# Kernel tuning notes

Hardware: AMD Instinct MI355X
Metric: run time of the kernel (lower is better)

The kernel has to match this reference:

```python
import jax, jax.numpy as jnp
import numpy as np

H, G, K = 8, 2, 16


def _sqdist(a, b):
    # a: [B,N,3], b: [B,M,3] -> [B,N,M] squared euclidean distances
    return ((a * a).sum(-1)[..., None] + (b * b).sum(-1)[..., None, :]
            - 2.0 * jnp.einsum('bnc,bmc->bnm', a, b))


_gather = jax.vmap(lambda p, i: p[i])  # points [N,C], idx [...,] -> [..., C]


def setup_inputs() -> dict:
    key = jax.random.key(0)
    B, N, C = 4, 1024, 384
    ks = jax.random.split(key, 10)
    def w(k, shape):
        return (jax.random.normal(k, shape, jnp.float32) / np.sqrt(shape[0]).astype(np.float32))
    return {
        'q': jax.random.normal(ks[0], (B, N, C), jnp.float32),
        'q_pos': jax.random.normal(ks[1], (B, N, 3), jnp.float32),
        'Wq': w(ks[2], (C, C)), 'Wk': w(ks[3], (C, C)), 'Wv': w(ks[4], (C, C)),
        'Wvoff': w(ks[5], (C, C)),
        'W_off1': w(ks[6], (C, C)),  # in = 2*group_dims = 2*(C//2) = C
        'b_off1': jnp.zeros((C,), jnp.float32),
        'ln_g': jnp.ones((C,), jnp.float32), 'ln_b': jnp.zeros((C,), jnp.float32),
        'W_off2': w(ks[7], (C, 3)),
        'Wp': w(ks[8], (C, C)), 'bp': jnp.zeros((C,), jnp.float32),
    }


def reference(q, q_pos, Wq, Wk, Wv, Wvoff, W_off1, b_off1, ln_g, ln_b, W_off2, Wp, bp):
    B, N, C = q.shape
    hd, gc = C // H, C // G
    scale_attn = hd ** -0.5
    v, v_pos = q, q_pos  # self-attention usage

    # --- kNN in 3D (topk smallest squared distances) ---
    d2 = _sqdist(q_pos, v_pos)                       # [B,N,N]
    _, idx = jax.lax.top_k(-d2, K)                    # [B,N,K]

    qp = q @ Wq                                       # [B,N,C]
    v_off = v @ Wvoff
    local_v = _gather(v_off, idx)                     # [B,N,K,C]

    # group split: 'b n k (g c) -> (b g) n k c'
    off_local_v = local_v.reshape(B, N, K, G, gc).transpose(0, 3, 1, 2, 4).reshape(B * G, N, K, gc)
    group_q = qp.reshape(B, N, G, gc).transpose(0, 2, 1, 3).reshape(B * G, N, gc)
    shift_feat = jnp.concatenate(
        [off_local_v, jnp.broadcast_to(group_q[:, :, None, :], (B * G, N, K, gc))], axis=-1)

    # --- offset MLP: Linear -> LayerNorm -> GELU -> Linear(no bias) -> tanh ---
    h = shift_feat @ W_off1 + b_off1
    mu = h.mean(-1, keepdims=True)
    var = ((h - mu) ** 2).mean(-1, keepdims=True)
    h = (h - mu) / jnp.sqrt(var + 1e-5) * ln_g + ln_b
    h = jax.nn.gelu(h, approximate=False)
    offset = jnp.tanh(h @ W_off2)                     # [(B G),N,K,3]

    # --- shift positions within local ball ---
    local_v_pos = _gather(v_pos, idx)                 # [B,N,K,3]
    local_v_pos = jnp.broadcast_to(local_v_pos[:, None], (B, G, N, K, 3)).reshape(B * G, N, K, 3)
    sc = (local_v_pos.max(-2) - local_v_pos.min(-2))[:, :, None, :] * 0.5
    shift_pos = (local_v_pos + offset * sc).reshape(B * G, N * K, 3)

    v_pos_g = jnp.broadcast_to(v_pos[:, None], (B, G, N, 3)).reshape(B * G, N, 3)
    v_g = v.reshape(B, N, G, gc).transpose(0, 2, 1, 3).reshape(B * G, N, gc)

    # --- three_nn + three_interpolate (inverse-distance weights over 3 NNs) ---
    d2n = _sqdist(shift_pos, v_pos_g)                 # [(B G), N*K, N]
    negd, idx3 = jax.lax.top_k(-d2n, 3)
    dist = jnp.sqrt(jnp.maximum(-negd, 0.0))          # three_nn returns euclidean dist
    recip = 1.0 / (dist + 1e-8)
    weight = recip / recip.sum(-1, keepdims=True)     # [(B G), N*K, 3]
    feats = _gather(v_g, idx3)                        # [(B G), N*K, 3, gc]
    interp = (feats * weight[..., None]).sum(-2)      # [(B G), N*K, gc]
    interp = interp.reshape(B, G, N, K, gc).transpose(0, 2, 3, 1, 4).reshape(B, N, K, C)

    # --- local cross-attn: 1 query token vs K interpolated keys/values ---
    kf = (interp @ Wk).reshape(B, N, K, H, hd)
    vf = (interp @ Wv).reshape(B, N, K, H, hd)
    qh = qp.reshape(B, N, H, hd)
    attn = jnp.einsum('bnhc,bnkhc->bnhk', qh, kf) * scale_attn
    attn = jax.nn.softmax(attn, axis=-1)
    out = jnp.einsum('bnhk,bnkhc->bnhc', attn, vf).reshape(B, N, C)
    return out @ Wp + bp
```

## Files before the change

kernel.cpp:

```cpp
#include <hip/hip_runtime.h>
#include <math.h>


#define ATTN_SCALE 0.14433756729740643f

#define OFF_IDX   0u
#define OFF_SC    65536u
#define OFF_QP    77824u
#define OFF_VOFF  1650688u
#define OFF_P     3223552u
#define OFF_Q     6369280u
#define OFF_SP    9515008u
#define OFF_W3    9908224u
#define OFF_I3    10301440u
#define OFF_QKH   10694656u
#define OFF_VW    23277568u
#define OFF_OPRE  35860480u

__device__ __forceinline__ float fast_erff(float z) {
  float az = fabsf(z);
  float d = fmaf(0.3275911f, az, 1.0f);
  float t0 = __builtin_amdgcn_rcpf(d);
  float t = t0 * fmaf(-d, t0, 2.0f);
  float e = __builtin_amdgcn_exp2f(z * z * -1.4426950408889634f);
  float p = fmaf(fmaf(fmaf(fmaf(1.061405429f, t, -1.453152027f),
                           t, 1.421413741f),
                      t, -0.284496736f),
                 t, 0.254829592f);
  float r = 1.0f - p * t * e;
  return __builtin_copysignf(r, z);
}

__global__ __launch_bounds__(64) void knn_kernel(const float* __restrict__ qpos,
                                                 int* __restrict__ idx_out,
                                                 float* __restrict__ sc_out) {
  int bn = blockIdx.x;
  int b = bn >> 10, n = bn & 1023;
  int lane = threadIdx.x;
  const float* pb = qpos + (size_t)b * 1024 * 3;
  float qx = pb[n * 3 + 0], qy = pb[n * 3 + 1], qz = pb[n * 3 + 2];
  float qq = qx * qx + qy * qy + qz * qz;
  float d2[16];
#pragma unroll
  for (int u = 0; u < 16; ++u) {
    int p = lane + 64 * u;
    float px = pb[p * 3 + 0], py = pb[p * 3 + 1], pz = pb[p * 3 + 2];
    float pp = px * px + py * py + pz * pz;
    float dt = qx * px + qy * py + qz * pz;
    d2[u] = (qq + pp) - 2.0f * dt;
  }
  float mnx = 3.4e38f, mny = 3.4e38f, mnz = 3.4e38f;
  float mxx = -3.4e38f, mxy = -3.4e38f, mxz = -3.4e38f;
  for (int r = 0; r < 16; ++r) {
    float best = d2[0]; int bu = 0;
#pragma unroll
    for (int u = 1; u < 16; ++u) { if (d2[u] < best) { best = d2[u]; bu = u; } }
    int bidx = lane + 64 * bu;
#pragma unroll
    for (int off = 32; off > 0; off >>= 1) {
      float ov = __shfl_xor(best, off);
      int oi = __shfl_xor(bidx, off);
      if (ov < best || (ov == best && oi < bidx)) { best = ov; bidx = oi; }
    }
    if ((bidx & 63) == lane) d2[bidx >> 6] = 3.4e38f;
    float wx = pb[bidx * 3 + 0], wy = pb[bidx * 3 + 1], wz = pb[bidx * 3 + 2];
    mnx = fminf(mnx, wx); mny = fminf(mny, wy); mnz = fminf(mnz, wz);
    mxx = fmaxf(mxx, wx); mxy = fmaxf(mxy, wy); mxz = fmaxf(mxz, wz);
    if (lane == 0) idx_out[bn * 16 + r] = bidx;
  }
  if (lane == 0) {
    sc_out[bn * 3 + 0] = 0.5f * (mxx - mnx);
    sc_out[bn * 3 + 1] = 0.5f * (mxy - mny);
    sc_out[bn * 3 + 2] = 0.5f * (mxz - mnz);
  }
}

__global__ __launch_bounds__(256) void gemm_qp_voff(const float* __restrict__ Aq,
    const float* __restrict__ W1, const float* __restrict__ W2,
    float* __restrict__ O1, float* __restrict__ O2) {
  __shared__ float As[16 * 132];
  __shared__ float Bs1[16 * 64];
  __shared__ float Bs2[16 * 64];
  int tid = threadIdx.x;
  int m0 = blockIdx.x * 128, n0 = blockIdx.y * 64;
  int arow = tid >> 1, akq = (tid & 1) * 8;
  int lk = tid >> 4, ln4 = (tid & 15) * 4;
  int tx = tid & 15, ty = tid >> 4;
  float a11[4][4] = {{0.f}}, a21[4][4] = {{0.f}};
  float a12[4][4] = {{0.f}}, a22[4][4] = {{0.f}};
  for (int k0 = 0; k0 < 384; k0 += 16) {
    float4 a0 = *(const float4*)(Aq + (size_t)(m0 + arow) * 384 + k0 + akq);
    float4 a1 = *(const float4*)(Aq + (size_t)(m0 + arow) * 384 + k0 + akq + 4);
    float4 b1 = *(const float4*)(W1 + (size_t)(k0 + lk) * 384 + n0 + ln4);
    float4 b2 = *(const float4*)(W2 + (size_t)(k0 + lk) * 384 + n0 + ln4);
    __syncthreads();
    As[(akq + 0) * 132 + arow] = a0.x; As[(akq + 1) * 132 + arow] = a0.y;
    As[(akq + 2) * 132 + arow] = a0.z; As[(akq + 3) * 132 + arow] = a0.w;
    As[(akq + 4) * 132 + arow] = a1.x; As[(akq + 5) * 132 + arow] = a1.y;
    As[(akq + 6) * 132 + arow] = a1.z; As[(akq + 7) * 132 + arow] = a1.w;
    *(float4*)(Bs1 + lk * 64 + ln4) = b1;
    *(float4*)(Bs2 + lk * 64 + ln4) = b2;
    __syncthreads();
#pragma unroll
    for (int k = 0; k < 16; ++k) {
      float4 av0 = *(const float4*)(As + k * 132 + ty * 4);
      float4 av1 = *(const float4*)(As + k * 132 + 64 + ty * 4);
      float4 bv1 = *(const float4*)(Bs1 + k * 64 + tx * 4);
      float4 bv2 = *(const float4*)(Bs2 + k * 64 + tx * 4);
      float x0[4] = {av0.x, av0.y, av0.z, av0.w};
      float x1[4] = {av1.x, av1.y, av1.z, av1.w};
      float c1[4] = {bv1.x, bv1.y, bv1.z, bv1.w};
      float c2[4] = {bv2.x, bv2.y, bv2.z, bv2.w};
#pragma unroll
      for (int i = 0; i < 4; ++i)
#pragma unroll
        for (int j = 0; j < 4; ++j) {
          a11[i][j] = fmaf(x0[i], c1[j], a11[i][j]);
          a21[i][j] = fmaf(x1[i], c1[j], a21[i][j]);
          a12[i][j] = fmaf(x0[i], c2[j], a12[i][j]);
          a22[i][j] = fmaf(x1[i], c2[j], a22[i][j]);
        }
    }
  }
#pragma unroll
  for (int i = 0; i < 4; ++i) {
    size_t rA = (size_t)(m0 + ty * 4 + i);
    size_t rB = (size_t)(m0 + 64 + ty * 4 + i);
    *(float4*)(O1 + rA * 384 + n0 + tx * 4) = make_float4(a11[i][0], a11[i][1], a11[i][2], a11[i][3]);
    *(float4*)(O1 + rB * 384 + n0 + tx * 4) = make_float4(a21[i][0], a21[i][1], a21[i][2], a21[i][3]);
    *(float4*)(O2 + rA * 384 + n0 + tx * 4) = make_float4(a12[i][0], a12[i][1], a12[i][2], a12[i][3]);
    *(float4*)(O2 + rB * 384 + n0 + tx * 4) = make_float4(a22[i][0], a22[i][1], a22[i][2], a22[i][3]);
  }
}

__global__ __launch_bounds__(256) void gemm_pq3(const float* __restrict__ voff,
    const float* __restrict__ qp, const float* __restrict__ qin,
    const float* __restrict__ Woff1, const float* __restrict__ boff1,
    const float* __restrict__ Wv,
    float* __restrict__ P, float* __restrict__ Q, float* __restrict__ VW) {
  __shared__ float As[16 * 132];
  __shared__ float Bs[16 * 64];
  int tid = threadIdx.x;
  int m0 = blockIdx.x * 128, n0 = blockIdx.y * 64, z = blockIdx.z;
  int bg = m0 >> 10; int b = bg >> 1; int g = bg & 1; int ml0 = m0 & 1023;
  const float* Abase; const float* Bbase; const float* bias; float* Out; int bog;
  if (z == 0)      { Abase = voff; Bbase = Woff1;             bias = nullptr; Out = P;  bog = 0; }
  else if (z == 1) { Abase = qp;   Bbase = Woff1 + 192 * 384; bias = boff1;   Out = Q;  bog = 0; }
  else             { Abase = qin;  Bbase = Wv;                bias = nullptr; Out = VW; bog = 192 * 384; }
  const float* A = Abase + (size_t)b * 1024 * 384 + g * 192;
  const float* B = Bbase + (size_t)g * bog;
  int arow = tid >> 1, akq = (tid & 1) * 8;
  int lk = tid >> 4, ln4 = (tid & 15) * 4;
  int tx = tid & 15, ty = tid >> 4;
  float accA[4][4] = {{0.f}}, accB[4][4] = {{0.f}};
  for (int k0 = 0; k0 < 192; k0 += 16) {
    float4 a0 = *(const float4*)(A + (size_t)(ml0 + arow) * 384 + k0 + akq);
    float4 a1 = *(const float4*)(A + (size_t)(ml0 + arow) * 384 + k0 + akq + 4);
    float4 b4 = *(const float4*)(B + (size_t)(k0 + lk) * 384 + n0 + ln4);
    __syncthreads();
    As[(akq + 0) * 132 + arow] = a0.x; As[(akq + 1) * 132 + arow] = a0.y;
    As[(akq + 2) * 132 + arow] = a0.z; As[(akq + 3) * 132 + arow] = a0.w;
    As[(akq + 4) * 132 + arow] = a1.x; As[(akq + 5) * 132 + arow] = a1.y;
    As[(akq + 6) * 132 + arow] = a1.z; As[(akq + 7) * 132 + arow] = a1.w;
    *(float4*)(Bs + lk * 64 + ln4) = b4;
    __syncthreads();
#pragma unroll
    for (int k = 0; k < 16; ++k) {
      float4 av0 = *(const float4*)(As + k * 132 + ty * 4);
      float4 av1 = *(const float4*)(As + k * 132 + 64 + ty * 4);
      float4 bv = *(const float4*)(Bs + k * 64 + tx * 4);
      float a0v[4] = {av0.x, av0.y, av0.z, av0.w};
      float a1v[4] = {av1.x, av1.y, av1.z, av1.w};
      float c[4] = {bv.x, bv.y, bv.z, bv.w};
#pragma unroll
      for (int i = 0; i < 4; ++i)
#pragma unroll
        for (int j = 0; j < 4; ++j) {
          accA[i][j] = fmaf(a0v[i], c[j], accA[i][j]);
          accB[i][j] = fmaf(a1v[i], c[j], accB[i][j]);
        }
    }
  }
  float bb[4] = {0.f, 0.f, 0.f, 0.f};
  if (bias) {
    bb[0] = bias[n0 + tx * 4 + 0]; bb[1] = bias[n0 + tx * 4 + 1];
    bb[2] = bias[n0 + tx * 4 + 2]; bb[3] = bias[n0 + tx * 4 + 3];
  }
#pragma unroll
  for (int i = 0; i < 4; ++i) {
    size_t rowA = (size_t)(m0 + ty * 4 + i);
    size_t rowB = (size_t)(m0 + 64 + ty * 4 + i);
    *(float4*)(Out + rowA * 384 + n0 + tx * 4) =
        make_float4(accA[i][0] + bb[0], accA[i][1] + bb[1], accA[i][2] + bb[2], accA[i][3] + bb[3]);
    *(float4*)(Out + rowB * 384 + n0 + tx * 4) =
        make_float4(accB[i][0] + bb[0], accB[i][1] + bb[1], accB[i][2] + bb[2], accB[i][3] + bb[3]);
  }
}

__global__ __launch_bounds__(256) void offset_assemble(const float* __restrict__ P,
    const float* __restrict__ Q, const int* __restrict__ idx,
    const float* __restrict__ lng, const float* __restrict__ lnb,
    const float* __restrict__ W2, const float* __restrict__ qpos,
    const float* __restrict__ sc, float* __restrict__ sp) {
  int row = blockIdx.x * 4 + (threadIdx.x >> 6);
  int lane = threadIdx.x & 63;
  int k = row & 15, n = (row >> 4) & 1023, bg = row >> 14;
  int b = bg >> 1;
  int mi = idx[((b << 10) + n) * 16 + k];
  const float* Pr = P + ((size_t)bg * 1024 + mi) * 384;
  const float* Qr = Q + ((size_t)bg * 1024 + n) * 384;
  float h[6]; float s = 0.f, s2 = 0.f;
#pragma unroll
  for (int u = 0; u < 3; ++u) {
    int c = 2 * lane + 128 * u;
    float2 pv = *(const float2*)(Pr + c);
    float2 qv = *(const float2*)(Qr + c);
    float h0 = pv.x + qv.x, h1 = pv.y + qv.y;
    h[2 * u] = h0; h[2 * u + 1] = h1;
    s += h0 + h1;
    s2 = fmaf(h0, h0, s2);
    s2 = fmaf(h1, h1, s2);
  }
#pragma unroll
  for (int off = 32; off > 0; off >>= 1) {
    s  += __shfl_xor(s, off);
    s2 += __shfl_xor(s2, off);
  }
  float mu = s * (1.0f / 384.0f);
  float var = s2 * (1.0f / 384.0f) - mu * mu;
  float rstd = 1.0f / sqrtf(var + 1e-5f);
  float o0 = 0.f, o1 = 0.f, o2 = 0.f;
#pragma unroll
  for (int u = 0; u < 3; ++u) {
    int c = 2 * lane + 128 * u;
    float2 gv  = *(const float2*)(lng + c);
    float2 bv  = *(const float2*)(lnb + c);
    float2 w01 = *(const float2*)(W2 + (size_t)c * 3);
    float2 w23 = *(const float2*)(W2 + (size_t)c * 3 + 2);
    float2 w45 = *(const float2*)(W2 + (size_t)c * 3 + 4);
    float x0 = fmaf((h[2 * u] - mu) * rstd, gv.x, bv.x);
    float x1 = fmaf((h[2 * u + 1] - mu) * rstd, gv.y, bv.y);
    float g0 = x0 * fmaf(fast_erff(x0 * 0.70710678118654752f), 0.5f, 0.5f);
    float g1 = x1 * fmaf(fast_erff(x1 * 0.70710678118654752f), 0.5f, 0.5f);
    o0 = fmaf(g0, w01.x, o0); o1 = fmaf(g0, w01.y, o1); o2 = fmaf(g0, w23.x, o2);
    o0 = fmaf(g1, w23.y, o0); o1 = fmaf(g1, w45.x, o1); o2 = fmaf(g1, w45.y, o2);
  }
#pragma unroll
  for (int off = 32; off > 0; off >>= 1) {
    o0 += __shfl_xor(o0, off);
    o1 += __shfl_xor(o1, off);
    o2 += __shfl_xor(o2, off);
  }
  if (lane < 3) {
    float o = (lane == 0) ? o0 : ((lane == 1) ? o1 : o2);
    float off = tanhf(o);
    float p = qpos[((size_t)b * 1024 + mi) * 3 + lane];
    float scv = sc[((b << 10) + n) * 3 + lane];
    sp[(size_t)row * 3 + lane] = p + off * scv;
  }
}

__global__ __launch_bounds__(256) void three_nn_kernel(const float* __restrict__ spos,
    const float* __restrict__ qpos, float* __restrict__ w3, int* __restrict__ i3) {
  __shared__ float px[1024], py[1024], pz[1024], pp[1024];
  int bg = blockIdx.x >> 5;
  int m0 = (blockIdx.x & 31) * 512;
  int b = bg >> 1;
  const float* pb = qpos + (size_t)b * 1024 * 3;
  for (int j = threadIdx.x; j < 1024; j += 256) {
    float x = pb[j * 3 + 0], y = pb[j * 3 + 1], z = pb[j * 3 + 2];
    px[j] = x; py[j] = y; pz[j] = z; pp[j] = x * x + y * y + z * z;
  }
  __syncthreads();
  int mA = m0 + threadIdx.x;
  int mB = mA + 256;
  const float* spA = spos + ((size_t)bg * 16384 + mA) * 3;
  const float* spB = spos + ((size_t)bg * 16384 + mB) * 3;
  float sxA = spA[0], syA = spA[1], szA = spA[2];
  float sxB = spB[0], syB = spB[1], szB = spB[2];
  float qqA = sxA * sxA + syA * syA + szA * szA;
  float qqB = sxB * sxB + syB * syB + szB * szB;
  float d0A = 3.4e38f, d1A = 3.4e38f, d2A = 3.4e38f;
  int i0A = 0, i1A = 0, i2A = 0;
  float d0B = 3.4e38f, d1B = 3.4e38f, d2B = 3.4e38f;
  int i0B = 0, i1B = 0, i2B = 0;
#pragma unroll 8
  for (int j = 0; j < 1024; ++j) {
    float cx = px[j], cy = py[j], cz = pz[j], cw = pp[j];
    float dtA = sxA * cx + syA * cy + szA * cz;
    float dA = (qqA + cw) - 2.0f * dtA;
    float dtB = sxB * cx + syB * cy + szB * cz;
    float dB = (qqB + cw) - 2.0f * dtB;
    {
      bool c0 = dA < d0A, c1 = dA < d1A, c2 = dA < d2A;
      float nd2 = c1 ? d1A : (c2 ? dA : d2A);
      int   ni2 = c1 ? i1A : (c2 ? j : i2A);
      float nd1 = c0 ? d0A : (c1 ? dA : d1A);
      int   ni1 = c0 ? i0A : (c1 ? j : i1A);
      d0A = c0 ? dA : d0A;  i0A = c0 ? j : i0A;
      d1A = nd1; i1A = ni1; d2A = nd2; i2A = ni2;
    }
    {
      bool c0 = dB < d0B, c1 = dB < d1B, c2 = dB < d2B;
      float nd2 = c1 ? d1B : (c2 ? dB : d2B);
      int   ni2 = c1 ? i1B : (c2 ? j : i2B);
      float nd1 = c0 ? d0B : (c1 ? dB : d1B);
      int   ni1 = c0 ? i0B : (c1 ? j : i1B);
      d0B = c0 ? dB : d0B;  i0B = c0 ? j : i0B;
      d1B = nd1; i1B = ni1; d2B = nd2; i2B = ni2;
    }
  }
  {
    float t0 = sqrtf(fmaxf(d0A, 0.f)), t1 = sqrtf(fmaxf(d1A, 0.f)), t2 = sqrtf(fmaxf(d2A, 0.f));
    float r0 = 1.0f / (t0 + 1e-8f), r1 = 1.0f / (t1 + 1e-8f), r2 = 1.0f / (t2 + 1e-8f);
    float inv = 1.0f / (r0 + r1 + r2);
    size_t base = ((size_t)bg * 16384 + mA) * 3;
    w3[base + 0] = r0 * inv; w3[base + 1] = r1 * inv; w3[base + 2] = r2 * inv;
    i3[base + 0] = i0A; i3[base + 1] = i1A; i3[base + 2] = i2A;
  }
  {
    float t0 = sqrtf(fmaxf(d0B, 0.f)), t1 = sqrtf(fmaxf(d1B, 0.f)), t2 = sqrtf(fmaxf(d2B, 0.f));
    float r0 = 1.0f / (t0 + 1e-8f), r1 = 1.0f / (t1 + 1e-8f), r2 = 1.0f / (t2 + 1e-8f);
    float inv = 1.0f / (r0 + r1 + r2);
    size_t base = ((size_t)bg * 16384 + mB) * 3;
    w3[base + 0] = r0 * inv; w3[base + 1] = r1 * inv; w3[base + 2] = r2 * inv;
    i3[base + 0] = i0B; i3[base + 1] = i1B; i3[base + 2] = i2B;
  }
}

__global__ __launch_bounds__(256) void gemm_qkh(const float* __restrict__ qp,
    const float* __restrict__ Wk, float* __restrict__ qkh) {
  __shared__ float As[16 * 132];
  __shared__ float Bs[16 * 68];
  int tid = threadIdx.x;
  int m0 = blockIdx.x * 128, c0 = blockIdx.y * 64, h = blockIdx.z;
  int arow = tid >> 1, akq = (tid & 1) * 8;
  int lm = tid >> 2, lq = (tid & 3) * 4;
  int tx = tid & 15, ty = tid >> 4;
  float accA[4][4] = {{0.f}}, accB[4][4] = {{0.f}};
  for (int k0 = 0; k0 < 48; k0 += 16) {
    float4 a0 = *(const float4*)(qp + (size_t)(m0 + arow) * 384 + h * 48 + k0 + akq);
    float4 a1 = *(const float4*)(qp + (size_t)(m0 + arow) * 384 + h * 48 + k0 + akq + 4);
    float4 b4 = *(const float4*)(Wk + (size_t)(c0 + lm) * 384 + h * 48 + k0 + lq);
    __syncthreads();
    As[(akq + 0) * 132 + arow] = a0.x; As[(akq + 1) * 132 + arow] = a0.y;
    As[(akq + 2) * 132 + arow] = a0.z; As[(akq + 3) * 132 + arow] = a0.w;
    As[(akq + 4) * 132 + arow] = a1.x; As[(akq + 5) * 132 + arow] = a1.y;
    As[(akq + 6) * 132 + arow] = a1.z; As[(akq + 7) * 132 + arow] = a1.w;
    Bs[(lq + 0) * 68 + lm] = b4.x; Bs[(lq + 1) * 68 + lm] = b4.y;
    Bs[(lq + 2) * 68 + lm] = b4.z; Bs[(lq + 3) * 68 + lm] = b4.w;
    __syncthreads();
#pragma unroll
    for (int k = 0; k < 16; ++k) {
      float4 av0 = *(const float4*)(As + k * 132 + ty * 4);
      float4 av1 = *(const float4*)(As + k * 132 + 64 + ty * 4);
      float4 bv = *(const float4*)(Bs + k * 68 + tx * 4);
      float a0v[4] = {av0.x, av0.y, av0.z, av0.w};
      float a1v[4] = {av1.x, av1.y, av1.z, av1.w};
      float c[4] = {bv.x, bv.y, bv.z, bv.w};
#pragma unroll
      for (int i = 0; i < 4; ++i)
#pragma unroll
        for (int j = 0; j < 4; ++j) {
          accA[i][j] = fmaf(a0v[i], c[j], accA[i][j]);
          accB[i][j] = fmaf(a1v[i], c[j], accB[i][j]);
        }
    }
  }
#pragma unroll
  for (int i = 0; i < 4; ++i) {
    size_t rowA = (size_t)(m0 + ty * 4 + i);
    size_t rowB = (size_t)(m0 + 64 + ty * 4 + i);
    *(float4*)(qkh + (rowA * 8 + h) * 384 + c0 + tx * 4) =
        make_float4(accA[i][0], accA[i][1], accA[i][2], accA[i][3]);
    *(float4*)(qkh + (rowB * 8 + h) * 384 + c0 + tx * 4) =
        make_float4(accB[i][0], accB[i][1], accB[i][2], accB[i][3]);
  }
}

__global__ __launch_bounds__(256) void attn_fuse2(const float* __restrict__ v,
    const float* __restrict__ w3, const int* __restrict__ i3,
    const float* __restrict__ qkh, const float* __restrict__ VW,
    float* __restrict__ opre) {
  __shared__ float A[16 * 388];
  __shared__ float Bv[16 * 388];
  __shared__ float wk[16][2][3];
  __shared__ int ik[16][2][3];
  __shared__ float attnw[8 * 16];
  __shared__ float lpart[2][128];
  int tid = threadIdx.x;
  int blk = blockIdx.x;
  int b = (blk & 7) >> 1;
  int n = ((blk & 1) << 9) | (blk >> 3);
  int bn = (b << 10) | n;
  if (tid < 96) {
    int k = tid / 6; int rem = tid % 6; int g = rem / 3; int s = rem % 3;
    size_t base = ((size_t)(b * 2 + g) * 16384 + n * 16 + k) * 3 + s;
    wk[k][g][s] = w3[base];
    ik[k][g][s] = i3[base];
  }
  __syncthreads();
  {
    int r = tid >> 4;
    int cL = (tid & 15) * 4;
    const float* vr[2][3]; const float* wr[2][3];
#pragma unroll
    for (int g = 0; g < 2; ++g)
#pragma unroll
      for (int s = 0; s < 3; ++s) {
        vr[g][s] = v + ((size_t)b * 1024 + ik[r][g][s]) * 384;
        wr[g][s] = VW + ((size_t)(b * 2 + g) * 1024 + ik[r][g][s]) * 384;
      }
    float u0 = wk[r][0][0], u1 = wk[r][0][1], u2 = wk[r][0][2];
    float y0 = wk[r][1][0], y1 = wk[r][1][1], y2 = wk[r][1][2];
#pragma unroll
    for (int u = 0; u < 6; ++u) {
      int c = cL + 64 * u;
      int g = (u >= 3) ? 1 : 0;
      float w0 = wk[r][g][0], w1 = wk[r][g][1], w2 = wk[r][g][2];
      float4 f0 = *(const float4*)(vr[g][0] + c);
      float4 f1 = *(const float4*)(vr[g][1] + c);
      float4 f2 = *(const float4*)(vr[g][2] + c);
      float4 o;
      o.x = w0 * f0.x + w1 * f1.x + w2 * f2.x;
      o.y = w0 * f0.y + w1 * f1.y + w2 * f2.y;
      o.z = w0 * f0.z + w1 * f1.z + w2 * f2.z;
      o.w = w0 * f0.w + w1 * f1.w + w2 * f2.w;
      *(float4*)(A + r * 388 + c) = o;
      float4 a0 = *(const float4*)(wr[0][0] + c);
      float4 a1 = *(const float4*)(wr[0][1] + c);
      float4 a2 = *(const float4*)(wr[0][2] + c);
      float4 b0 = *(const float4*)(wr[1][0] + c);
      float4 b1 = *(const float4*)(wr[1][1] + c);
      float4 b2 = *(const float4*)(wr[1][2] + c);
      float4 p;
      p.x = u0 * a0.x + u1 * a1.x + u2 * a2.x + y0 * b0.x + y1 * b1.x + y2 * b2.x;
      p.y = u0 * a0.y + u1 * a1.y + u2 * a2.y + y0 * b0.y + y1 * b1.y + y2 * b2.y;
      p.z = u0 * a0.z + u1 * a1.z + u2 * a2.z + y0 * b0.z + y1 * b1.z + y2 * b2.z;
      p.w = u0 * a0.w + u1 * a1.w + u2 * a2.w + y0 * b0.w + y1 * b1.w + y2 * b2.w;
      *(float4*)(Bv + r * 388 + c) = p;
    }
  }
  __syncthreads();
  {
    int r = tid & 15, h = (tid >> 4) & 7, half = tid >> 7;
    const float* qr = qkh + ((size_t)bn * 8 + h) * 384 + half * 192;
    const float* ar = A + r * 388 + half * 192;
    float acc = 0.f;
    for (int c = 0; c < 192; c += 4) {
      float4 av = *(const float4*)(ar + c);
      float4 qv = *(const float4*)(qr + c);
      acc += av.x * qv.x + av.y * qv.y + av.z * qv.z + av.w * qv.w;
    }
    lpart[half][h * 16 + r] = acc;
  }
  __syncthreads();
  if (tid < 128) attnw[tid] = (lpart[0][tid] + lpart[1][tid]) * ATTN_SCALE;
  __syncthreads();
  if (tid < 8) {
    int h = tid;
    float m = -3.4e38f;
    for (int k = 0; k < 16; ++k) m = fmaxf(m, attnw[h * 16 + k]);
    float s = 0.f;
    for (int k = 0; k < 16; ++k) { float e = expf(attnw[h * 16 + k] - m); attnw[h * 16 + k] = e; s += e; }
    float inv = 1.0f / s;
    for (int k = 0; k < 16; ++k) attnw[h * 16 + k] *= inv;
  }
  __syncthreads();
  {
#pragma unroll
    for (int u = 0; u < 2; ++u) {
      int c = tid + 256 * u;
      if (c < 384) {
        int h = c / 48;
        float s = 0.f;
#pragma unroll
        for (int k = 0; k < 16; ++k) s = fmaf(attnw[h * 16 + k], Bv[k * 388 + c], s);
        opre[(size_t)bn * 384 + c] = s;
      }
    }
  }
}

__global__ __launch_bounds__(256) void gemm_final(const float* __restrict__ Ain,
    const float* __restrict__ Wp, const float* __restrict__ bp,
    float* __restrict__ Out) {
  __shared__ float As[16 * 132];
  __shared__ float Bs[16 * 64];
  int tid = threadIdx.x;
  int m0 = blockIdx.x * 128, n0 = blockIdx.y * 64;
  int arow = tid >> 1, akq = (tid & 1) * 8;
  int lk = tid >> 4, ln4 = (tid & 15) * 4;
  int tx = tid & 15, ty = tid >> 4;
  float accA[4][4] = {{0.f}}, accB[4][4] = {{0.f}};
  for (int k0 = 0; k0 < 384; k0 += 16) {
    float4 a0 = *(const float4*)(Ain + (size_t)(m0 + arow) * 384 + k0 + akq);
    float4 a1 = *(const float4*)(Ain + (size_t)(m0 + arow) * 384 + k0 + akq + 4);
    float4 b4 = *(const float4*)(Wp + (size_t)(k0 + lk) * 384 + n0 + ln4);
    __syncthreads();
    As[(akq + 0) * 132 + arow] = a0.x; As[(akq + 1) * 132 + arow] = a0.y;
    As[(akq + 2) * 132 + arow] = a0.z; As[(akq + 3) * 132 + arow] = a0.w;
    As[(akq + 4) * 132 + arow] = a1.x; As[(akq + 5) * 132 + arow] = a1.y;
    As[(akq + 6) * 132 + arow] = a1.z; As[(akq + 7) * 132 + arow] = a1.w;
    *(float4*)(Bs + lk * 64 + ln4) = b4;
    __syncthreads();
#pragma unroll
    for (int k = 0; k < 16; ++k) {
      float4 av0 = *(const float4*)(As + k * 132 + ty * 4);
      float4 av1 = *(const float4*)(As + k * 132 + 64 + ty * 4);
      float4 bv = *(const float4*)(Bs + k * 64 + tx * 4);
      float a0v[4] = {av0.x, av0.y, av0.z, av0.w};
      float a1v[4] = {av1.x, av1.y, av1.z, av1.w};
      float c[4] = {bv.x, bv.y, bv.z, bv.w};
#pragma unroll
      for (int i = 0; i < 4; ++i)
#pragma unroll
        for (int j = 0; j < 4; ++j) {
          accA[i][j] = fmaf(a0v[i], c[j], accA[i][j]);
          accB[i][j] = fmaf(a1v[i], c[j], accB[i][j]);
        }
    }
  }
  float bb[4];
  bb[0] = bp[n0 + tx * 4 + 0]; bb[1] = bp[n0 + tx * 4 + 1];
  bb[2] = bp[n0 + tx * 4 + 2]; bb[3] = bp[n0 + tx * 4 + 3];
#pragma unroll
  for (int i = 0; i < 4; ++i) {
    size_t rowA = (size_t)(m0 + ty * 4 + i);
    size_t rowB = (size_t)(m0 + 64 + ty * 4 + i);
    *(float4*)(Out + rowA * 384 + n0 + tx * 4) =
        make_float4(accA[i][0] + bb[0], accA[i][1] + bb[1], accA[i][2] + bb[2], accA[i][3] + bb[3]);
    *(float4*)(Out + rowB * 384 + n0 + tx * 4) =
        make_float4(accB[i][0] + bb[0], accB[i][1] + bb[1], accB[i][2] + bb[2], accB[i][3] + bb[3]);
  }
}

extern "C" void kernel_launch(void* const* d_in, const int* in_sizes, int n_in,
                              void* d_out, int out_size, void* d_ws, size_t ws_size,
                              hipStream_t stream) {
  (void)in_sizes; (void)n_in; (void)out_size; (void)ws_size;
  const float* q     = (const float*)d_in[0];
  const float* qpos  = (const float*)d_in[1];
  const float* Wq    = (const float*)d_in[2];
  const float* Wk    = (const float*)d_in[3];
  const float* Wv    = (const float*)d_in[4];
  const float* Wvoff = (const float*)d_in[5];
  const float* Woff1 = (const float*)d_in[6];
  const float* boff1 = (const float*)d_in[7];
  const float* lng   = (const float*)d_in[8];
  const float* lnb   = (const float*)d_in[9];
  const float* Woff2 = (const float*)d_in[10];
  const float* Wp    = (const float*)d_in[11];
  const float* bp    = (const float*)d_in[12];
  float* out = (float*)d_out;
  float* ws = (float*)d_ws;
  int*   idxb = (int*)(ws + OFF_IDX);
  float* sc   = ws + OFF_SC;
  float* qp   = ws + OFF_QP;
  float* voff = ws + OFF_VOFF;
  float* P    = ws + OFF_P;
  float* Q    = ws + OFF_Q;
  float* spos = ws + OFF_SP;
  float* w3   = ws + OFF_W3;
  int*   i3   = (int*)(ws + OFF_I3);
  float* qkh  = ws + OFF_QKH;
  float* VW   = ws + OFF_VW;
  float* opre = ws + OFF_OPRE;

  knn_kernel<<<4096, 64, 0, stream>>>(qpos, idxb, sc);
  gemm_qp_voff<<<dim3(32, 6), 256, 0, stream>>>(q, Wq, Wvoff, qp, voff);
  gemm_pq3<<<dim3(64, 6, 3), 256, 0, stream>>>(voff, qp, q, Woff1, boff1, Wv, P, Q, VW);
  offset_assemble<<<32768, 256, 0, stream>>>(P, Q, idxb, lng, lnb, Woff2, qpos, sc, spos);
  three_nn_kernel<<<256, 256, 0, stream>>>(spos, qpos, w3, i3);
  gemm_qkh<<<dim3(32, 6, 8), 256, 0, stream>>>(qp, Wk, qkh);
  attn_fuse2<<<4096, 256, 0, stream>>>(q, w3, i3, qkh, VW, opre);
  gemm_final<<<dim3(32, 6), 256, 0, stream>>>(opre, Wp, bp, out);
}
```

Measured before the change: 493.4 us.

## Split three-NN search across candidate chunks with a separate merge kernel

The three-nearest-neighbour search is split four ways over the 1024 candidate points. Each block scans only 256 candidates and writes partial top-3 distances and indices into scratch space reused from the P buffer. A second kernel merges the four partial top-3 lists and computes the inverse-distance weights. This raises the grid from 256 to 1024 blocks to fill more compute units, at the cost of an extra launch and partial-result traffic. Reusing the P region is only safe if P is no longer needed at this point.

```diff
diff --git a/kernel.cpp b/kernel.cpp
--- a/kernel.cpp
+++ b/kernel.cpp
@@ -16,6 +16,8 @@
 #define OFF_QKH   10694656u
 #define OFF_VW    23277568u
 #define OFF_OPRE  35860480u
+#define OFF_P3D   OFF_P
+#define OFF_P3I   (OFF_P + 1572864u)
 
 __device__ __forceinline__ float fast_erff(float z) {
   float az = fabsf(z);
@@ -260,18 +262,24 @@
   }
 }
 
-__global__ __launch_bounds__(256) void three_nn_kernel(const float* __restrict__ spos,
-    const float* __restrict__ qpos, float* __restrict__ w3, int* __restrict__ i3) {
-  __shared__ float px[1024], py[1024], pz[1024], pp[1024];
-  int bg = blockIdx.x >> 5;
-  int m0 = (blockIdx.x & 31) * 512;
+__global__ __launch_bounds__(256) void three_nn_part(const float* __restrict__ spos,
+    const float* __restrict__ qpos, float* __restrict__ part_d, int* __restrict__ part_i) {
+  __shared__ float px[256], py[256], pz[256], pp[256];
+  int bid = blockIdx.x;
+  int bg = bid >> 7;
+  int qg = (bid >> 2) & 31;
+  int c  = bid & 3;
   int b = bg >> 1;
+  int j0 = c << 8;
   const float* pb = qpos + (size_t)b * 1024 * 3;
-  for (int j = threadIdx.x; j < 1024; j += 256) {
+  {
+    int jj = threadIdx.x;
+    int j = j0 + jj;
     float x = pb[j * 3 + 0], y = pb[j * 3 + 1], z = pb[j * 3 + 2];
-    px[j] = x; py[j] = y; pz[j] = z; pp[j] = x * x + y * y + z * z;
+    px[jj] = x; py[jj] = y; pz[jj] = z; pp[jj] = x * x + y * y + z * z;
   }
   __syncthreads();
+  int m0 = qg * 512;
   int mA = m0 + threadIdx.x;
   int mB = mA + 256;
   const float* spA = spos + ((size_t)bg * 16384 + mA) * 3;
@@ -285,8 +293,9 @@
   float d0B = 3.4e38f, d1B = 3.4e38f, d2B = 3.4e38f;
   int i0B = 0, i1B = 0, i2B = 0;
 #pragma unroll 8
-  for (int j = 0; j < 1024; ++j) {
-    float cx = px[j], cy = py[j], cz = pz[j], cw = pp[j];
+  for (int jj = 0; jj < 256; ++jj) {
+    int j = j0 + jj;
+    float cx = px[jj], cy = py[jj], cz = pz[jj], cw = pp[jj];
     float dtA = sxA * cx + syA * cy + szA * cz;
     float dA = (qqA + cw) - 2.0f * dtA;
     float dtB = sxB * cx + syB * cy + szB * cz;
@@ -311,21 +320,46 @@
     }
   }
   {
-    float t0 = sqrtf(fmaxf(d0A, 0.f)), t1 = sqrtf(fmaxf(d1A, 0.f)), t2 = sqrtf(fmaxf(d2A, 0.f));
-    float r0 = 1.0f / (t0 + 1e-8f), r1 = 1.0f / (t1 + 1e-8f), r2 = 1.0f / (t2 + 1e-8f);
-    float inv = 1.0f / (r0 + r1 + r2);
-    size_t base = ((size_t)bg * 16384 + mA) * 3;
-    w3[base + 0] = r0 * inv; w3[base + 1] = r1 * inv; w3[base + 2] = r2 * inv;
-    i3[base + 0] = i0A; i3[base + 1] = i1A; i3[base + 2] = i2A;
+    size_t base = (((size_t)bg * 4 + c) * 16384 + mA) * 3;
+    part_d[base + 0] = d0A; part_d[base + 1] = d1A; part_d[base + 2] = d2A;
+    part_i[base + 0] = i0A; part_i[base + 1] = i1A; part_i[base + 2] = i2A;
   }
   {
-    float t0 = sqrtf(fmaxf(d0B, 0.f)), t1 = sqrtf(fmaxf(d1B, 0.f)), t2 = sqrtf(fmaxf(d2B, 0.f));
-    float r0 = 1.0f / (t0 + 1e-8f), r1 = 1.0f / (t1 + 1e-8f), r2 = 1.0f / (t2 + 1e-8f);
-    float inv = 1.0f / (r0 + r1 + r2);
-    size_t base = ((size_t)bg * 16384 + mB) * 3;
-    w3[base + 0] = r0 * inv; w3[base + 1] = r1 * inv; w3[base + 2] = r2 * inv;
-    i3[base + 0] = i0B; i3[base + 1] = i1B; i3[base + 2] = i2B;
-  }
+    size_t base = (((size_t)bg * 4 + c) * 16384 + mB) * 3;
+    part_d[base + 0] = d0B; part_d[base + 1] = d1B; part_d[base + 2] = d2B;
+    part_i[base + 0] = i0B; part_i[base + 1] = i1B; part_i[base + 2] = i2B;
+  }
+}
+
+__global__ __launch_bounds__(256) void three_nn_merge(const float* __restrict__ part_d,
+    const int* __restrict__ part_i, float* __restrict__ w3, int* __restrict__ i3) {
+  int q = blockIdx.x * 256 + threadIdx.x;
+  int bg = q >> 14, m = q & 16383;
+  size_t pb = (((size_t)bg * 4) * 16384 + m) * 3;
+  float D0 = part_d[pb + 0], D1 = part_d[pb + 1], D2 = part_d[pb + 2];
+  int   I0 = part_i[pb + 0], I1 = part_i[pb + 1], I2 = part_i[pb + 2];
+#pragma unroll
+  for (int c = 1; c < 4; ++c) {
+    size_t base = (((size_t)bg * 4 + c) * 16384 + m) * 3;
+#pragma unroll
+    for (int s = 0; s < 3; ++s) {
+      float dv = part_d[base + s];
+      int   iv = part_i[base + s];
+      bool c0 = dv < D0, c1 = dv < D1, c2 = dv < D2;
+      float nd2 = c1 ? D1 : (c2 ? dv : D2);
+      int   ni2 = c1 ? I1 : (c2 ? iv : I2);
+      float nd1 = c0 ? D0 : (c1 ? dv : D1);
+      int   ni1 = c0 ? I0 : (c1 ? iv : I1);
+      D0 = c0 ? dv : D0;  I0 = c0 ? iv : I0;
+      D1 = nd1; I1 = ni1; D2 = nd2; I2 = ni2;
+    }
+  }
+  float t0 = sqrtf(fmaxf(D0, 0.f)), t1 = sqrtf(fmaxf(D1, 0.f)), t2 = sqrtf(fmaxf(D2, 0.f));
+  float r0 = 1.0f / (t0 + 1e-8f), r1 = 1.0f / (t1 + 1e-8f), r2 = 1.0f / (t2 + 1e-8f);
+  float inv = 1.0f / (r0 + r1 + r2);
+  size_t base = ((size_t)bg * 16384 + m) * 3;
+  w3[base + 0] = r0 * inv; w3[base + 1] = r1 * inv; w3[base + 2] = r2 * inv;
+  i3[base + 0] = I0; i3[base + 1] = I1; i3[base + 2] = I2;
 }
 
 __global__ __launch_bounds__(256) void gemm_qkh(const float* __restrict__ qp,
@@ -566,12 +600,15 @@
   float* qkh  = ws + OFF_QKH;
   float* VW   = ws + OFF_VW;
   float* opre = ws + OFF_OPRE;
+  float* p3d  = ws + OFF_P3D;
+  int*   p3i  = (int*)(ws + OFF_P3I);
 
   knn_kernel<<<4096, 64, 0, stream>>>(qpos, idxb, sc);
   gemm_qp_voff<<<dim3(32, 6), 256, 0, stream>>>(q, Wq, Wvoff, qp, voff);
   gemm_pq3<<<dim3(64, 6, 3), 256, 0, stream>>>(voff, qp, q, Woff1, boff1, Wv, P, Q, VW);
   offset_assemble<<<32768, 256, 0, stream>>>(P, Q, idxb, lng, lnb, Woff2, qpos, sc, spos);
-  three_nn_kernel<<<256, 256, 0, stream>>>(spos, qpos, w3, i3);
+  three_nn_part<<<1024, 256, 0, stream>>>(spos, qpos, p3d, p3i);
+  three_nn_merge<<<512, 256, 0, stream>>>(p3d, p3i, w3, i3);
   gemm_qkh<<<dim3(32, 6, 8), 256, 0, stream>>>(qp, Wk, qkh);
   attn_fuse2<<<4096, 256, 0, stream>>>(q, w3, i3, qkh, VW, opre);
   gemm_final<<<dim3(32, 6), 256, 0, stream>>>(opre, Wp, bp, out);
```

New measurement: 479.9 us. 2.7% less time.
